# Performance work log

Hardware: AMD Instinct MI355X
Metric: run time of the kernel (lower is better)

## Reference

```python
import jax, jax.numpy as jnp
import numpy as np

N_NODES = 50000
N_EDGES = 500000
IN_CH = 128
OUT_CH = 64
HEADS = 4


def setup_inputs() -> dict:
    key = jax.random.key(0)
    ks = jax.random.split(key, 9)
    x = jax.random.normal(ks[0], (N_NODES, IN_CH), dtype=jnp.float32)
    edge_index = jax.random.randint(ks[1], (2, N_EDGES), 0, N_NODES, dtype=jnp.int64)
    edge_weights = jax.random.uniform(ks[2], (N_EDGES, 1), dtype=jnp.float32)
    # xavier-uniform params, stored as [in, out] so y = x @ W
    def xavier(k, shape):
        fan_in, fan_out = shape
        lim = float(np.sqrt(6.0 / (fan_in + fan_out)))
        return jax.random.uniform(k, shape, minval=-lim, maxval=lim, dtype=jnp.float32)
    Wq = xavier(ks[3], (IN_CH, OUT_CH * HEADS))
    Wk = xavier(ks[4], (IN_CH, OUT_CH * HEADS))
    Wv = xavier(ks[5], (IN_CH, OUT_CH * HEADS))
    We = xavier(ks[6], (1, HEADS))
    Wout = xavier(ks[7], (OUT_CH * HEADS, OUT_CH))
    b_out = jnp.zeros((OUT_CH,), dtype=jnp.float32)
    return {"x": x, "edge_index": edge_index, "edge_weights": edge_weights,
            "Wq": Wq, "Wk": Wk, "Wv": Wv, "We": We, "Wout": Wout, "b_out": b_out}


def reference(x, edge_index, edge_weights, Wq, Wk, Wv, We, Wout, b_out):
    num_nodes = x.shape[0]
    src = edge_index[0]
    tgt = edge_index[1]
    x_src = x[src]                                    # [E, in]
    x_tgt = x[tgt]                                    # [E, in]
    q = (x_tgt @ Wq).reshape(-1, HEADS, OUT_CH)       # [E, H, C]
    k = (x_src @ Wk).reshape(-1, HEADS, OUT_CH)
    v = (x_src @ Wv).reshape(-1, HEADS, OUT_CH)
    attn = jnp.sum(q * k, axis=-1) / jnp.sqrt(jnp.float32(OUT_CH))  # [E, H]
    attn = attn + edge_weights @ We                   # [E, H]
    attn = jax.nn.leaky_relu(attn, negative_slope=0.2)
    attn = jax.nn.softmax(attn, axis=0)               # global softmax over edges (as in source)
    weighted_v = attn[..., None] * v                  # [E, H, C]
    out = jax.ops.segment_sum(weighted_v, tgt, num_segments=num_nodes)  # [N, H, C]
    out = out.reshape(num_nodes, HEADS * OUT_CH) @ Wout + b_out         # [N, out]
    if x.shape == out.shape:
        out = out + x
    return out
```

## Files before the change

kernel.cpp:

```cpp
#include <hip/hip_runtime.h>
#include <hip/hip_bf16.h>
#include <hip/hip_fp16.h>

#define N_NODES 50000
#define N_EDGES 500000
#define IN_CH   128
#define D       256
#define UDIM    512
#define OUT_CH  64
#define HEADS   4
#define NC      49
#define PCAP    1024

#define NB_X16  6250
#define NB_HIST 1954
#define NB_MB   256
#define NB_ZB   128
#define NB_GEMM 1564
#define NB_SCAT 1954

typedef _Float16 half8 __attribute__((ext_vector_type(8)));
typedef _Float16 half2_t __attribute__((ext_vector_type(2)));
typedef float   floatx4 __attribute__((ext_vector_type(4)));

__global__ __launch_bounds__(256) void k1_prep_kernel(const float* __restrict__ x,
                                                      __half* __restrict__ x16,
                                                      const int* __restrict__ ei,
                                                      int* __restrict__ cnt,
                                                      double* __restrict__ S,
                                                      const float* __restrict__ Wq,
                                                      const float* __restrict__ Wk,
                                                      const float* __restrict__ Wv,
                                                      const float* __restrict__ Wout,
                                                      __half* __restrict__ M16t,
                                                      __half* __restrict__ Zc16t) {
    __shared__ float sbuf[4][64];
    const int b = blockIdx.x, tid = threadIdx.x;
    if (b < NB_X16) {
        int i = b * 256 + tid;
        if (i < HEADS) S[i] = 0.0;
        int k = i * 4;
        if (k < N_NODES * IN_CH) {
            float4 v = *(const float4*)(x + k);
            union { __half2 h[2]; uint2 u; } pk;
            pk.h[0] = __floats2half2_rn(v.x, v.y);
            pk.h[1] = __floats2half2_rn(v.z, v.w);
            *(uint2*)(x16 + k) = pk.u;
        }
    } else if (b < NB_X16 + NB_HIST) {
        int e = (b - NB_X16) * 256 + tid;
        if (e < N_EDGES) atomicAdd(&cnt[ei[N_EDGES + e]], 1);
    } else if (b < NB_X16 + NB_HIST + NB_MB) {
        const int r = (b - NB_X16 - NB_HIST) * 2 + (tid >> 7);
        const int i = tid & 127;
        const int h = r >> 7, j = r & 127;
        float* buf = sbuf[tid >> 7];
        if (i < 64) buf[i] = Wk[(size_t)j * D + h * 64 + i];
        __syncthreads();
        const float4* qr = (const float4*)(Wq + (size_t)i * D + h * 64);
        float s = 0.f;
        #pragma unroll
        for (int c4 = 0; c4 < 16; ++c4) {
            float4 q = qr[c4];
            s += q.x * buf[c4 * 4] + q.y * buf[c4 * 4 + 1]
               + q.z * buf[c4 * 4 + 2] + q.w * buf[c4 * 4 + 3];
        }
        M16t[(size_t)r * IN_CH + i] = __float2half(s);
    } else {
        const int r = (b - NB_X16 - NB_HIST - NB_MB) * 4 + (tid >> 6);
        const int c = tid & 63;
        const int h = r >> 7, i = r & 127;
        float* buf = sbuf[tid >> 6];
        buf[c] = Wv[(size_t)i * D + h * 64 + c];
        __syncthreads();
        float s = 0.f;
        #pragma unroll 8
        for (int j = 0; j < 64; ++j)
            s += buf[j] * Wout[(size_t)(h * 64 + j) * OUT_CH + c];
        Zc16t[(size_t)c * UDIM + r] = __float2half(s);
    }
}

__global__ __launch_bounds__(256) void k2_scan_reduce_kernel(const int* __restrict__ cnt,
                                                             int* __restrict__ csum) {
    const int b = blockIdx.x, tid = threadIdx.x;
    const int lane = tid & 63, wid = tid >> 6;
    int s = 0;
    int idx0 = b * 1024 + tid * 4;
    #pragma unroll
    for (int i = 0; i < 4; ++i) {
        int idx = idx0 + i;
        if (idx < N_NODES) s += cnt[idx];
    }
    #pragma unroll
    for (int m = 1; m < 64; m <<= 1) s += __shfl_xor(s, m, 64);
    __shared__ int w4[4];
    if (lane == 0) w4[wid] = s;
    __syncthreads();
    if (tid == 0) csum[b] = w4[0] + w4[1] + w4[2] + w4[3];
}

__global__ __launch_bounds__(256) void k3_scan_chunks_kernel(int* __restrict__ cnt,
                                                             const int* __restrict__ csum,
                                                             int* __restrict__ rp) {
    __shared__ int stop[64];
    __shared__ int wsum[4];
    const int b = blockIdx.x, tid = threadIdx.x;
    const int lane = tid & 63, wid = tid >> 6;
    if (tid < 64) stop[tid] = (tid < NC) ? csum[tid] : 0;
    __syncthreads();
    int base = 0;
    for (int w = 0; w < b; ++w) base += stop[w];
    int v[4];
    const int idx0 = b * 1024 + tid * 4;
    #pragma unroll
    for (int i = 0; i < 4; ++i) {
        int idx = idx0 + i;
        v[i] = (idx < N_NODES) ? cnt[idx] : 0;
    }
    int tsum = v[0] + v[1] + v[2] + v[3];
    int x = tsum;
    #pragma unroll
    for (int d = 1; d < 64; d <<= 1) {
        int y = __shfl_up(x, d, 64);
        if (lane >= d) x += y;
    }
    if (lane == 63) wsum[wid] = x;
    __syncthreads();
    int woff = 0;
    for (int w = 0; w < wid; ++w) woff += wsum[w];
    int excl = base + woff + x - tsum;
    #pragma unroll
    for (int i = 0; i < 4; ++i) {
        int idx = idx0 + i;
        if (idx < N_NODES) { rp[idx] = excl; cnt[idx] = excl; }
        excl += v[i];
    }
}

__global__ __launch_bounds__(256) void k4_gemmu_scatter_kernel(const __half* __restrict__ x16,
                                                               const __half* __restrict__ M16t,
                                                               __half* __restrict__ u16,
                                                               const int* __restrict__ ei,
                                                               const float* __restrict__ ew,
                                                               int* __restrict__ cnt,
                                                               int2* __restrict__ payload) {
    __shared__ __half Bm[128][136];
    const int tid = threadIdx.x;
    if (blockIdx.x >= NB_GEMM) {
        int e = (blockIdx.x - NB_GEMM) * 256 + tid;
        if (e < N_EDGES) {
            int s = ei[e], t = ei[N_EDGES + e];
            int pos = atomicAdd(&cnt[t], 1);
            payload[pos] = make_int2(s, __float_as_int(ew[e]));
        }
        return;
    }
    const int m0 = (blockIdx.x % 391) * 128;
    const int colbase = (blockIdx.x / 391) * 128;
    {
        const int r = tid >> 1, part = tid & 1;
        const uint4* sb = (const uint4*)(M16t + (size_t)(colbase + r) * IN_CH + part * 64);
        uint4* db = (uint4*)&Bm[r][part * 64];
        #pragma unroll
        for (int q = 0; q < 8; ++q) db[q] = sb[q];
    }

    const int w = tid >> 6, lane = tid & 63;
    const int mrow = lane & 15, quad = lane >> 4;

    half8 a[2][4];
    #pragma unroll
    for (int mt = 0; mt < 2; ++mt) {
        int row = min(m0 + w * 32 + mt * 16 + mrow, N_NODES - 1);
        const __half* ab = x16 + (size_t)row * IN_CH + quad * 8;
        #pragma unroll
        for (int ks = 0; ks < 4; ++ks) a[mt][ks] = *(const half8*)(ab + ks * 32);
    }
    __syncthreads();

    floatx4 acc[2][8];
    #pragma unroll
    for (int mt = 0; mt < 2; ++mt)
        #pragma unroll
        for (int nt = 0; nt < 8; ++nt)
            acc[mt][nt] = (floatx4){0.f, 0.f, 0.f, 0.f};

    #pragma unroll
    for (int nt = 0; nt < 8; ++nt) {
        #pragma unroll
        for (int ks = 0; ks < 4; ++ks) {
            half8 bfr = *(const half8*)&Bm[nt * 16 + mrow][ks * 32 + quad * 8];
            acc[0][nt] = __builtin_amdgcn_mfma_f32_16x16x32_f16(a[0][ks], bfr, acc[0][nt], 0, 0, 0);
            acc[1][nt] = __builtin_amdgcn_mfma_f32_16x16x32_f16(a[1][ks], bfr, acc[1][nt], 0, 0, 0);
        }
    }
    __syncthreads();
    #pragma unroll
    for (int mt = 0; mt < 2; ++mt)
        #pragma unroll
        for (int nt = 0; nt < 8; ++nt)
            #pragma unroll
            for (int r = 0; r < 4; ++r)
                Bm[w * 32 + mt * 16 + quad * 4 + r][nt * 16 + mrow] = __float2half(acc[mt][nt][r]);
    __syncthreads();
    {
        const int r = tid >> 1, part = tid & 1;
        if (m0 + r < N_NODES) {
            const uint4* s4 = (const uint4*)&Bm[r][part * 64];
            uint4* d4 = (uint4*)(u16 + (size_t)(m0 + r) * UDIM + colbase + part * 64);
            #pragma unroll
            for (int q = 0; q < 8; ++q) d4[q] = s4[q];
        }
    }
}

__global__ __launch_bounds__(256) void edge_fused_kernel(const __half* __restrict__ u16,
                                                         const __half* __restrict__ x16,
                                                         const int* __restrict__ rp,
                                                         const int* __restrict__ cnt,
                                                         const int2* __restrict__ payload,
                                                         const float* __restrict__ We,
                                                         __half* __restrict__ y16,
                                                         double* __restrict__ S) {
    __shared__ int2 pbuf[PCAP];
    __shared__ float sblk[4];
    const int tid = threadIdx.x;
    const int nodebase = blockIdx.x * 16;

    const int span0 = rp[nodebase];
    const int span1 = cnt[nodebase + 15];
    const int span_len = min(span1 - span0, PCAP);
    for (int i = tid; i < span_len; i += 256) pbuf[i] = payload[span0 + i];
    if (tid < 4) sblk[tid] = 0.f;
    __syncthreads();

    const int l16 = tid & 15;
    const int h = l16 >> 2;
    const int q = l16 & 3;
    const int node = nodebase + (tid >> 4);
    const float wev = We[h];

    uint4 ur4[4];
    {
        const uint4* ub = (const uint4*)(u16 + (size_t)node * UDIM + h * 128 + q * 32);
        ur4[0] = ub[0]; ur4[1] = ub[1]; ur4[2] = ub[2]; ur4[3] = ub[3];
    }
    const half2_t* uh = (const half2_t*)ur4;

    half2_t yacc[16];
    #pragma unroll
    for (int t = 0; t < 16; ++t) yacc[t] = (half2_t){(_Float16)0.f, (_Float16)0.f};

    float sacc = 0.f;
    const int start = rp[node];
    const int end = cnt[node];

    auto getpl = [&](int e) -> int2 {
        int idx = e - span0;
        return (idx < PCAP) ? pbuf[idx] : payload[e];
    };

    int2 pl = make_int2(0, 0);
    uint4 xr[4];
    if (start < end) {
        pl = getpl(start);
        const uint4* xb = (const uint4*)(x16 + (size_t)pl.x * IN_CH + q * 32);
        xr[0] = xb[0]; xr[1] = xb[1]; xr[2] = xb[2]; xr[3] = xb[3];
    }
    for (int e = start; e < end; ++e) {
        int2 pln = pl;
        uint4 xrn[4] = {xr[0], xr[1], xr[2], xr[3]};
        if (e + 1 < end) {
            pln = getpl(e + 1);
            const uint4* xb = (const uint4*)(x16 + (size_t)pln.x * IN_CH + q * 32);
            xrn[0] = xb[0]; xrn[1] = xb[1]; xrn[2] = xb[2]; xrn[3] = xb[3];
        }
        const half2_t* xh = (const half2_t*)xr;
        float dot = 0.f;
        #pragma unroll
        for (int t = 0; t < 16; ++t)
            dot = __builtin_amdgcn_fdot2(uh[t], xh[t], dot, false);
        dot += __shfl_xor(dot, 1, 16);
        dot += __shfl_xor(dot, 2, 16);
        float l = dot * 0.125f + __int_as_float(pl.y) * wev;
        l = fmaxf(l, 0.2f * l);
        float p = __expf(l);
        if (q == 0) sacc += p;
        half2_t p2 = (half2_t){(_Float16)p, (_Float16)p};
        #pragma unroll
        for (int t = 0; t < 16; ++t)
            yacc[t] = p2 * xh[t] + yacc[t];
        pl = pln;
        xr[0] = xrn[0]; xr[1] = xrn[1]; xr[2] = xrn[2]; xr[3] = xrn[3];
    }
    {
        uint4* yo = (uint4*)(y16 + (size_t)node * UDIM + h * 128 + q * 32);
        const uint4* ys = (const uint4*)yacc;
        yo[0] = ys[0]; yo[1] = ys[1]; yo[2] = ys[2]; yo[3] = ys[3];
    }
    __syncthreads();
    if (q == 0) atomicAdd(&sblk[h], sacc);
    __syncthreads();
    if (tid < 4) atomicAdd(&S[tid], (double)sblk[tid]);
}

__global__ __launch_bounds__(256) void gemm_out_mfma_kernel(const __half* __restrict__ y16,
                                                            const __half* __restrict__ Zc16t,
                                                            const double* __restrict__ S,
                                                            const float* __restrict__ b_out,
                                                            float* __restrict__ out) {
    __shared__ __half Ay[128][136];
    __shared__ __half Bz[64][136];
    __shared__ float invs_s[4];
    const int m0 = blockIdx.x * 128;
    const int tid = threadIdx.x;
    if (tid < 4) invs_s[tid] = (float)(1.0 / S[tid]);

    const int w = tid >> 6, lane = tid & 63;
    const int mrow = lane & 15, quad = lane >> 4;

    floatx4 result[2][4];
    #pragma unroll
    for (int mt = 0; mt < 2; ++mt)
        #pragma unroll
        for (int nt = 0; nt < 4; ++nt)
            result[mt][nt] = (floatx4){0.f, 0.f, 0.f, 0.f};

    for (int h = 0; h < HEADS; ++h) {
        {
            const int r = tid >> 1, part = tid & 1;
            uint4 va[8];
            if (m0 + r < N_NODES) {
                const uint4* src = (const uint4*)(y16 + (size_t)(m0 + r) * UDIM + h * 128 + part * 64);
                #pragma unroll
                for (int qq = 0; qq < 8; ++qq) va[qq] = src[qq];
            } else {
                #pragma unroll
                for (int qq = 0; qq < 8; ++qq) va[qq] = make_uint4(0u, 0u, 0u, 0u);
            }
            uint4* da = (uint4*)&Ay[r][part * 64];
            #pragma unroll
            for (int qq = 0; qq < 8; ++qq) da[qq] = va[qq];
        }
        {
            const int r = tid >> 2, part = tid & 3;
            const uint4* sb = (const uint4*)(Zc16t + (size_t)r * UDIM + h * 128 + part * 32);
            uint4* db = (uint4*)&Bz[r][part * 32];
            #pragma unroll
            for (int qq = 0; qq < 4; ++qq) db[qq] = sb[qq];
        }
        __syncthreads();

        half8 a[2][4];
        #pragma unroll
        for (int mt = 0; mt < 2; ++mt)
            #pragma unroll
            for (int ks = 0; ks < 4; ++ks)
                a[mt][ks] = *(const half8*)&Ay[w * 32 + mt * 16 + mrow][ks * 32 + quad * 8];

        floatx4 acc[2][4];
        #pragma unroll
        for (int mt = 0; mt < 2; ++mt)
            #pragma unroll
            for (int nt = 0; nt < 4; ++nt)
                acc[mt][nt] = (floatx4){0.f, 0.f, 0.f, 0.f};

        #pragma unroll
        for (int nt = 0; nt < 4; ++nt) {
            #pragma unroll
            for (int ks = 0; ks < 4; ++ks) {
                half8 bfr = *(const half8*)&Bz[nt * 16 + mrow][ks * 32 + quad * 8];
                acc[0][nt] = __builtin_amdgcn_mfma_f32_16x16x32_f16(a[0][ks], bfr, acc[0][nt], 0, 0, 0);
                acc[1][nt] = __builtin_amdgcn_mfma_f32_16x16x32_f16(a[1][ks], bfr, acc[1][nt], 0, 0, 0);
            }
        }
        const float inv = invs_s[h];
        #pragma unroll
        for (int mt = 0; mt < 2; ++mt)
            #pragma unroll
            for (int nt = 0; nt < 4; ++nt) {
                result[mt][nt][0] += inv * acc[mt][nt][0];
                result[mt][nt][1] += inv * acc[mt][nt][1];
                result[mt][nt][2] += inv * acc[mt][nt][2];
                result[mt][nt][3] += inv * acc[mt][nt][3];
            }
        __syncthreads();
    }
    float bcol[4];
    #pragma unroll
    for (int nt = 0; nt < 4; ++nt) bcol[nt] = b_out[nt * 16 + mrow];
    #pragma unroll
    for (int mt = 0; mt < 2; ++mt) {
        #pragma unroll
        for (int r = 0; r < 4; ++r) {
            int row = m0 + w * 32 + mt * 16 + quad * 4 + r;
            if (row < N_NODES) {
                float* dst = out + (size_t)row * OUT_CH;
                #pragma unroll
                for (int nt = 0; nt < 4; ++nt)
                    dst[nt * 16 + mrow] = result[mt][nt][r] + bcol[nt];
            }
        }
    }
}

extern "C" void kernel_launch(void* const* d_in, const int* in_sizes, int n_in,
                              void* d_out, int out_size, void* d_ws, size_t ws_size,
                              hipStream_t stream) {
    const float* x     = (const float*)d_in[0];
    const int*   ei    = (const int*)d_in[1];
    const float* ew    = (const float*)d_in[2];
    const float* Wq    = (const float*)d_in[3];
    const float* Wk    = (const float*)d_in[4];
    const float* Wv    = (const float*)d_in[5];
    const float* We    = (const float*)d_in[6];
    const float* Wout  = (const float*)d_in[7];
    const float* b_out = (const float*)d_in[8];
    float* out = (float*)d_out;

    __half* u16   = (__half*)d_ws;
    __half* y16   = u16 + (size_t)N_NODES * UDIM;
    __half* x16   = y16 + (size_t)N_NODES * UDIM;
    double* S     = (double*)(x16 + (size_t)N_NODES * IN_CH);
    __half* M16t  = (__half*)(S + HEADS);
    __half* Zc16t = M16t + UDIM * IN_CH;
    int*    rp    = (int*)(Zc16t + OUT_CH * UDIM);
    int*    cnt   = rp + N_NODES;
    int*    csum  = cnt + N_NODES;
    int2*   payload = (int2*)(csum + 64);

    hipMemsetAsync(cnt, 0, N_NODES * sizeof(int), stream);
    k1_prep_kernel<<<NB_X16 + NB_HIST + NB_MB + NB_ZB, 256, 0, stream>>>(
        x, x16, ei, cnt, S, Wq, Wk, Wv, Wout, M16t, Zc16t);
    k2_scan_reduce_kernel<<<NC, 256, 0, stream>>>(cnt, csum);
    k3_scan_chunks_kernel<<<NC, 256, 0, stream>>>(cnt, csum, rp);
    k4_gemmu_scatter_kernel<<<NB_GEMM + NB_SCAT, 256, 0, stream>>>(
        x16, M16t, u16, ei, ew, cnt, payload);
    edge_fused_kernel<<<N_NODES / 16, 256, 0, stream>>>(u16, x16, rp, cnt, payload, We, y16, S);
    gemm_out_mfma_kernel<<<(N_NODES + 127) / 128, 256, 0, stream>>>(y16, Zc16t, S, b_out, out);
}
```

Baseline: 253.3 us.

## Pipeline edge gathers through LDS ring with async global_load_lds prefetch

The edge loop now prefetches the gathered x16 rows DEPTH=4 edges ahead into a per-wave LDS ring buffer using global_load_lds, with explicit vmcnt waits and an XOR-swizzled chunk layout to avoid bank conflicts. Each wave iterates to the maximum degree across its four nodes and masks out inactive iterations. A fallback path keeps the old register double-buffered loop when a block's edge span exceeds the shrunken payload cache. The goal is to hide gather latency with deeper prefetch. In exchange, LDS use and wave-level divergence padding go up, and the hand-placed waitcnts must stay correct.

```diff
diff --git a/kernel.cpp b/kernel.cpp
--- a/kernel.cpp
+++ b/kernel.cpp
@@ -10,7 +10,8 @@
 #define OUT_CH  64
 #define HEADS   4
 #define NC      49
-#define PCAP    1024
+#define PCAP    768
+#define DEPTH   4
 
 #define NB_X16  6250
 #define NB_HIST 1954
@@ -22,6 +23,13 @@
 typedef _Float16 half8 __attribute__((ext_vector_type(8)));
 typedef _Float16 half2_t __attribute__((ext_vector_type(2)));
 typedef float   floatx4 __attribute__((ext_vector_type(4)));
+
+typedef __attribute__((address_space(1))) const void as1_void;
+typedef __attribute__((address_space(3))) void as3_void;
+
+__device__ __forceinline__ void gll16(const void* g, void* l) {
+    __builtin_amdgcn_global_load_lds((as1_void*)g, (as3_void*)l, 16, 0, 0);
+}
 
 __global__ __launch_bounds__(256) void k1_prep_kernel(const float* __restrict__ x,
                                                       __half* __restrict__ x16,
@@ -223,6 +231,7 @@
                                                          const float* __restrict__ We,
                                                          __half* __restrict__ y16,
                                                          double* __restrict__ S) {
+    __shared__ __half xring[4][DEPTH][512];
     __shared__ int2 pbuf[PCAP];
     __shared__ float sblk[4];
     const int tid = threadIdx.x;
@@ -230,12 +239,15 @@
 
     const int span0 = rp[nodebase];
     const int span1 = cnt[nodebase + 15];
-    const int span_len = min(span1 - span0, PCAP);
+    const int span  = span1 - span0;
+    const int span_len = min(span, PCAP);
     for (int i = tid; i < span_len; i += 256) pbuf[i] = payload[span0 + i];
     if (tid < 4) sblk[tid] = 0.f;
     __syncthreads();
 
-    const int l16 = tid & 15;
+    const int w = tid >> 6, lane = tid & 63;
+    const int g = lane >> 4;
+    const int l16 = lane & 15;
     const int h = l16 >> 2;
     const int q = l16 & 3;
     const int node = nodebase + (tid >> 4);
@@ -255,44 +267,101 @@
     float sacc = 0.f;
     const int start = rp[node];
     const int end = cnt[node];
-
-    auto getpl = [&](int e) -> int2 {
-        int idx = e - span0;
-        return (idx < PCAP) ? pbuf[idx] : payload[e];
-    };
-
-    int2 pl = make_int2(0, 0);
-    uint4 xr[4];
-    if (start < end) {
-        pl = getpl(start);
-        const uint4* xb = (const uint4*)(x16 + (size_t)pl.x * IN_CH + q * 32);
-        xr[0] = xb[0]; xr[1] = xb[1]; xr[2] = xb[2]; xr[3] = xb[3];
-    }
-    for (int e = start; e < end; ++e) {
-        int2 pln = pl;
-        uint4 xrn[4] = {xr[0], xr[1], xr[2], xr[3]};
-        if (e + 1 < end) {
-            pln = getpl(e + 1);
-            const uint4* xb = (const uint4*)(x16 + (size_t)pln.x * IN_CH + q * 32);
-            xrn[0] = xb[0]; xrn[1] = xb[1]; xrn[2] = xb[2]; xrn[3] = xb[3];
-        }
-        const half2_t* xh = (const half2_t*)xr;
-        float dot = 0.f;
-        #pragma unroll
-        for (int t = 0; t < 16; ++t)
-            dot = __builtin_amdgcn_fdot2(uh[t], xh[t], dot, false);
-        dot += __shfl_xor(dot, 1, 16);
-        dot += __shfl_xor(dot, 2, 16);
-        float l = dot * 0.125f + __int_as_float(pl.y) * wev;
-        l = fmaxf(l, 0.2f * l);
-        float p = __expf(l);
-        if (q == 0) sacc += p;
-        half2_t p2 = (half2_t){(_Float16)p, (_Float16)p};
-        #pragma unroll
-        for (int t = 0; t < 16; ++t)
-            yacc[t] = p2 * xh[t] + yacc[t];
-        pl = pln;
-        xr[0] = xrn[0]; xr[1] = xrn[1]; xr[2] = xrn[2]; xr[3] = xrn[3];
+    const int ng = end - start;
+
+    if (span <= PCAP) {
+        int nmax = ng;
+        nmax = max(nmax, __shfl_xor(nmax, 16, 64));
+        nmax = max(nmax, __shfl_xor(nmax, 32, 64));
+        if (nmax > 0) {
+            const int chunk_off = (l16 ^ g) * 8;
+            auto src_of = [&](int t) -> const __half* {
+                int idx = min(start + t, end - 1);
+                idx = max(idx, span0);
+                int s = pbuf[idx - span0].x;
+                return x16 + (size_t)s * IN_CH + chunk_off;
+            };
+            #pragma unroll
+            for (int s = 0; s < DEPTH; ++s)
+                gll16(src_of(s), &xring[w][s][0]);
+
+            for (int t = 0; t < nmax; ++t) {
+                const int slot = t & (DEPTH - 1);
+                asm volatile("s_waitcnt vmcnt(3)" ::: "memory");
+                __builtin_amdgcn_sched_barrier(0);
+                const uint4* rb = (const uint4*)&xring[w][slot][g * 128 + q * 32];
+                uint4 xr0 = rb[0 ^ g];
+                uint4 xr1 = rb[1 ^ g];
+                uint4 xr2 = rb[2 ^ g];
+                uint4 xr3 = rb[3 ^ g];
+                asm volatile("s_waitcnt lgkmcnt(0)" ::: "memory");
+                __builtin_amdgcn_sched_barrier(0);
+                gll16(src_of(t + DEPTH), &xring[w][slot][0]);
+
+                int2 pl;
+                {
+                    int idx = min(start + t, end - 1);
+                    idx = max(idx, span0);
+                    pl = pbuf[idx - span0];
+                }
+                uint4 xr[4] = {xr0, xr1, xr2, xr3};
+                const half2_t* xh = (const half2_t*)xr;
+                float dot = 0.f;
+                #pragma unroll
+                for (int tt = 0; tt < 16; ++tt)
+                    dot = __builtin_amdgcn_fdot2(uh[tt], xh[tt], dot, false);
+                dot += __shfl_xor(dot, 1, 16);
+                dot += __shfl_xor(dot, 2, 16);
+                float l = dot * 0.125f + __int_as_float(pl.y) * wev;
+                l = fmaxf(l, 0.2f * l);
+                float p = __expf(l);
+                if (t < ng) {
+                    if (q == 0) sacc += p;
+                    half2_t p2 = (half2_t){(_Float16)p, (_Float16)p};
+                    #pragma unroll
+                    for (int tt = 0; tt < 16; ++tt)
+                        yacc[tt] = p2 * xh[tt] + yacc[tt];
+                }
+            }
+        }
+    } else {
+        auto getpl = [&](int e) -> int2 {
+            int idx = e - span0;
+            return (idx < PCAP) ? pbuf[idx] : payload[e];
+        };
+        int2 pl = make_int2(0, 0);
+        uint4 xr[4];
+        if (start < end) {
+            pl = getpl(start);
+            const uint4* xb = (const uint4*)(x16 + (size_t)pl.x * IN_CH + q * 32);
+            xr[0] = xb[0]; xr[1] = xb[1]; xr[2] = xb[2]; xr[3] = xb[3];
+        }
+        for (int e = start; e < end; ++e) {
+            int2 pln = pl;
+            uint4 xrn[4] = {xr[0], xr[1], xr[2], xr[3]};
+            if (e + 1 < end) {
+                pln = getpl(e + 1);
+                const uint4* xb = (const uint4*)(x16 + (size_t)pln.x * IN_CH + q * 32);
+                xrn[0] = xb[0]; xrn[1] = xb[1]; xrn[2] = xb[2]; xrn[3] = xb[3];
+            }
+            const half2_t* xh = (const half2_t*)xr;
+            float dot = 0.f;
+            #pragma unroll
+            for (int t = 0; t < 16; ++t)
+                dot = __builtin_amdgcn_fdot2(uh[t], xh[t], dot, false);
+            dot += __shfl_xor(dot, 1, 16);
+            dot += __shfl_xor(dot, 2, 16);
+            float l = dot * 0.125f + __int_as_float(pl.y) * wev;
+            l = fmaxf(l, 0.2f * l);
+            float p = __expf(l);
+            if (q == 0) sacc += p;
+            half2_t p2 = (half2_t){(_Float16)p, (_Float16)p};
+            #pragma unroll
+            for (int t = 0; t < 16; ++t)
+                yacc[t] = p2 * xh[t] + yacc[t];
+            pl = pln;
+            xr[0] = xrn[0]; xr[1] = xrn[1]; xr[2] = xrn[2]; xr[3] = xrn[3];
+        }
     }
     {
         uint4* yo = (uint4*)(y16 + (size_t)node * UDIM + h * 128 + q * 32);
```

Result: faster. 239.6 us (-5.4%).
